# Kernel optimization log

Measured on AMD Instinct MI355X. Metric: run time of the kernel, lower is better.

Reference implementation:

```python
import jax, jax.numpy as jnp
import numpy as np

B, T = 64, 512
OBS, DM, DS, NL = 115, 128, 8, 3
EMB, NA, H1 = 16, 19, 256


def _ln(x, g, b, eps=1e-5):
    m = jnp.mean(x, -1, keepdims=True)
    v = jnp.mean((x - m) ** 2, -1, keepdims=True)
    return (x - m) * jax.lax.rsqrt(v + eps) * g + b


def _s6(x, h, lng, lnb, w_ig, w_dt, b_dt, a_log, w_b, w_c, d_par, w_out):
    # x: [B,T,DM], h: [B,DM,DS]
    xn = _ln(x, lng, lnb)
    xp = xn @ w_ig.T                               # [B,T,2*DM]
    x_in, z = xp[..., :DM], xp[..., DM:]
    dt = jax.nn.softplus(x_in @ w_dt.T + b_dt)     # [B,T,DM]
    A = -jnp.exp(a_log)                            # [DM,DS]
    bt = x_in @ w_b.T                              # [B,T,DS]
    ct = x_in @ w_c.T                              # [B,T,DS]
    dA = jnp.exp(dt[..., None] * A)                # [B,T,DM,DS]
    upd = (dt * x_in)[..., None] * bt[:, :, None, :]  # [B,T,DM,DS]

    def step(hc, inp):
        dA_t, u_t, c_t = inp
        hn = dA_t * hc + u_t                       # [B,DM,DS]
        y = jnp.einsum('bds,bs->bd', hn, c_t)      # [B,DM]
        return hn, y

    h_f, ys = jax.lax.scan(
        step, h,
        (jnp.swapaxes(dA, 0, 1), jnp.swapaxes(upd, 0, 1), jnp.swapaxes(ct, 0, 1)))
    y = jnp.swapaxes(ys, 0, 1)                     # [B,T,DM]
    ssm = y * jax.nn.silu(z) + x_in * d_par
    return x + ssm @ w_out.T, h_f.reshape(h_f.shape[0], -1)


def _forward(prev_actions, obs, h0, enc_w1, enc_b1, enc_g1, enc_bb1, enc_w2, enc_b2,
             enc_g2, enc_bb2, emb, proj_w, proj_b, proj_g, proj_bb,
             m_ln_g, m_ln_b, m_w_ig, m_w_dt, m_b_dt, m_a_log, m_w_b, m_w_c, m_d, m_w_out,
             fn_g, fn_b, pol_w1, pol_b1, pol_g, pol_bb, pol_w2, pol_b2):
    # MLP encoder: Linear -> LN -> SiLU -> Linear -> LN (final norm)
    e = jax.nn.silu(_ln(obs @ enc_w1.T + enc_b1, enc_g1, enc_bb1))
    e = _ln(e @ enc_w2.T + enc_b2, enc_g2, enc_bb2)
    pa = emb[prev_actions]                         # [B,T,EMB]
    x = jnp.concatenate([e, pa], -1) @ proj_w.T + proj_b
    x = jax.nn.silu(_ln(x, proj_g, proj_bb))
    for i in range(NL):
        x, _ = _s6(x, h0[i].reshape(-1, DM, DS), m_ln_g[i], m_ln_b[i], m_w_ig[i],
                   m_w_dt[i], m_b_dt[i], m_a_log[i], m_w_b[i], m_w_c[i], m_d[i], m_w_out[i])
    x = _ln(x, fn_g, fn_b)
    p = jax.nn.silu(_ln(x @ pol_w1.T + pol_b1, pol_g, pol_bb))
    return p @ pol_w2.T + pol_b2                   # [B,T,NA] policy logits


def setup_inputs() -> dict:
    key = jax.random.key(0)
    ks = iter(jax.random.split(key, 64))
    def n(shape, s=0.05):
        return jax.random.normal(next(ks), shape, dtype=jnp.float32) * s
    return {
        'obs': jax.random.normal(next(ks), (B, T, OBS), dtype=jnp.float32),
        'h0': jnp.zeros((NL, B, DM * DS), jnp.float32),
        'enc_w1': n((H1, OBS)), 'enc_b1': jnp.zeros((H1,)),
        'enc_g1': jnp.ones((H1,)), 'enc_bb1': jnp.zeros((H1,)),
        'enc_w2': n((DM, H1)), 'enc_b2': jnp.zeros((DM,)),
        'enc_g2': jnp.ones((DM,)), 'enc_bb2': jnp.zeros((DM,)),
        'emb': n((NA + 1, EMB), 1.0),
        'proj_w': n((DM, DM + EMB)), 'proj_b': jnp.zeros((DM,)),
        'proj_g': jnp.ones((DM,)), 'proj_bb': jnp.zeros((DM,)),
        'm_ln_g': jnp.ones((NL, DM)), 'm_ln_b': jnp.zeros((NL, DM)),
        'm_w_ig': n((NL, 2 * DM, DM)), 'm_w_dt': n((NL, DM, DM)),
        'm_b_dt': jnp.zeros((NL, DM)),
        'm_a_log': jax.random.uniform(next(ks), (NL, DM, DS), minval=-3.0, maxval=-1.0, dtype=jnp.float32),
        'm_w_b': n((NL, DS, DM)), 'm_w_c': n((NL, DS, DM)),
        'm_d': jnp.ones((NL, DM)), 'm_w_out': n((NL, DM, DM)),
        'fn_g': jnp.ones((DM,)), 'fn_b': jnp.zeros((DM,)),
        'pol_w1': n((DM, DM)), 'pol_b1': jnp.zeros((DM,)),
        'pol_g': jnp.ones((DM,)), 'pol_bb': jnp.zeros((DM,)),
        'pol_w2': n((NA, DM)), 'pol_b2': jnp.zeros((NA,)),
        'prev_actions': jax.random.randint(next(ks), (B, T), 0, NA + 1),
    }


def reference(obs, h0, enc_w1, enc_b1, enc_g1, enc_bb1, enc_w2, enc_b2, enc_g2, enc_bb2,
              emb, proj_w, proj_b, proj_g, proj_bb, m_ln_g, m_ln_b, m_w_ig, m_w_dt,
              m_b_dt, m_a_log, m_w_b, m_w_c, m_d, m_w_out, fn_g, fn_b, pol_w1, pol_b1,
              pol_g, pol_bb, pol_w2, pol_b2, prev_actions):
    return _forward(prev_actions, obs, h0, enc_w1, enc_b1, enc_g1, enc_bb1, enc_w2,
                    enc_b2, enc_g2, enc_bb2, emb, proj_w, proj_b, proj_g, proj_bb,
                    m_ln_g, m_ln_b, m_w_ig, m_w_dt, m_b_dt, m_a_log, m_w_b, m_w_c,
                    m_d, m_w_out, fn_g, fn_b, pol_w1, pol_b1, pol_g, pol_bb, pol_w2, pol_b2)
```

## Files before the change

### kernel.cpp

```cpp
#include <hip/hip_runtime.h>
#include <math.h>

#define BB 64
#define TT 512
#define OBSD 115
#define DMD 128
#define DSD 8
#define NLD 3
#define EMBD 16
#define NAD 19
#define H1D 256
#define NTOK (BB*TT)
#define SSEG 32
#define TSEG (TT/SSEG)

typedef unsigned short ushort_t;
typedef __attribute__((ext_vector_type(8))) short short8;
typedef __attribute__((ext_vector_type(4))) float f32x4;

__device__ __forceinline__ float silu_f(float x){ return x / (1.f + __expf(-x)); }
__device__ __forceinline__ float softplus_f(float x){
  return fmaxf(x, 0.f) + log1pf(__expf(-fabsf(x)));
}
__device__ __forceinline__ ushort_t f2bf(float x){
  unsigned u = __float_as_uint(x);
  unsigned r = (u + 0x7fffu + ((u >> 16) & 1u)) >> 16;
  return (ushort_t)r;
}
__device__ __forceinline__ float b2f(ushort_t x){
  return __uint_as_float(((unsigned)x) << 16);
}
#define MFMA(a,b,c) __builtin_amdgcn_mfma_f32_16x16x32_bf16((a),(b),(c),0,0,0)
#define LOG2E 1.44269504f

struct PJob { const float* src; ushort_t* dst; int N; int K; int Kpad; int rowofs; int Nw; };
struct PJobs { PJob j[20]; };

__global__ __launch_bounds__(256) void k_prep(PJobs P){
  const int job = blockIdx.x >> 2;
  const int sub = blockIdx.x & 3;
  PJob pj = P.j[job];
  const int elems = pj.Nw * pj.Kpad;
  for (int idx = sub*256 + threadIdx.x; idx < elems; idx += 4*256){
    int n = idx / pj.Kpad;
    int k = idx - n*pj.Kpad;
    float v = (n < pj.N && k < pj.K) ? pj.src[(size_t)n*pj.K + k] : 0.f;
    pj.dst[(size_t)(pj.rowofs + n)*pj.Kpad + k] = f2bf(v);
  }
}

__global__ __launch_bounds__(256, 6) void k_enc12p(
    const float* __restrict__ obs, const ushort_t* __restrict__ w1b,
    const float* __restrict__ b1, const float* __restrict__ g1,
    const float* __restrict__ bb1,
    const ushort_t* __restrict__ w2b,
    const float* __restrict__ b2, const float* __restrict__ g2,
    const float* __restrict__ bb2,
    const float* __restrict__ emb, const int* __restrict__ pact,
    const ushort_t* __restrict__ pwb, const float* __restrict__ pb,
    const float* __restrict__ pg, const float* __restrict__ pbb,
    float* __restrict__ X,
    const float* __restrict__ lng, const float* __restrict__ lnb,
    const ushort_t* __restrict__ wigb, const ushort_t* __restrict__ wdbcb,
    const float* __restrict__ bdt,
    ushort_t* __restrict__ XINb, ushort_t* __restrict__ Zb,
    ushort_t* __restrict__ DTb, ushort_t* __restrict__ BTu, ushort_t* __restrict__ CTu,
    const float* __restrict__ alog0,
    float* __restrict__ HLOC, float* __restrict__ PPR)
{
  __shared__ __align__(16) char sm[15104];
  ushort_t* s_obs = (ushort_t*)sm;
  ushort_t* s_e1  = (ushort_t*)sm;
  ushort_t* s_xin = (ushort_t*)sm;
  ushort_t* s_dt  = (ushort_t*)(sm + 4352);
  ushort_t* s_a2  = (ushort_t*)(sm + 8448);
  ushort_t* s_btc = (ushort_t*)(sm + 13824);
  float2*   s_st  = (float2*)(sm + 14080);
  float2*   s_st2 = (float2*)(sm + 14592);

  const int tok0 = blockIdx.x * 16;
  const int bidx = blockIdx.x >> 5;
  const int ch   = blockIdx.x & 31;
  const int tid = threadIdx.x;
  const int lane = tid & 63, w = tid >> 6;
  const int q = lane >> 4, cn = lane & 15;

  {
    const int t = tid >> 4, kc = tid & 15;
    const float* op = obs + (size_t)(tok0 + t)*OBSD;
    short8 v;
    #pragma unroll
    for (int j = 0; j < 8; j++){
      int k = kc*8 + j;
      v[j] = (short)f2bf(k < OBSD ? op[k] : 0.f);
    }
    *(short8*)&s_obs[t*136 + kc*8] = v;
  }
  for (int e = tid; e < 16*32; e += 256){
    int t = e >> 5, k = e & 31;
    float v = 0.f;
    if (k < EMBD){ int a = pact[tok0 + t]; v = emb[(size_t)a*EMBD + k]; }
    s_a2[t*168 + 128 + k] = f2bf(v);
  }
  __syncthreads();

  f32x4 acc[4];
  {
    short8 af[4];
    #pragma unroll
    for (int ks = 0; ks < 4; ks++)
      af[ks] = *(const short8*)&s_obs[cn*136 + ks*32 + q*8];
    #pragma unroll
    for (int nt = 0; nt < 4; nt++){
      const int n0 = (w*4 + nt) * 16;
      f32x4 a = {0.f,0.f,0.f,0.f};
      #pragma unroll
      for (int ks = 0; ks < 4; ks++){
        short8 bf = *(const short8*)&w1b[(size_t)(n0 + cn)*128 + ks*32 + q*8];
        a = MFMA(af[ks], bf, a);
      }
      float bv = b1[n0 + cn];
      #pragma unroll
      for (int r = 0; r < 4; r++) a[r] += bv;
      acc[nt] = a;
    }
    #pragma unroll
    for (int r = 0; r < 4; r++){
      float s = 0.f, s2 = 0.f;
      #pragma unroll
      for (int nt = 0; nt < 4; nt++){ float v = acc[nt][r]; s += v; s2 = fmaf(v, v, s2); }
      s += __shfl_xor(s, 1, 64); s2 += __shfl_xor(s2, 1, 64);
      s += __shfl_xor(s, 2, 64); s2 += __shfl_xor(s2, 2, 64);
      s += __shfl_xor(s, 4, 64); s2 += __shfl_xor(s2, 4, 64);
      s += __shfl_xor(s, 8, 64); s2 += __shfl_xor(s2, 8, 64);
      if (cn == 0) s_st[(q*4 + r)*4 + w] = make_float2(s, s2);
    }
  }
  __syncthreads();

  {
    float mu[4], rs[4];
    #pragma unroll
    for (int r = 0; r < 4; r++){
      const int row = q*4 + r;
      float2 p0 = s_st[row*4+0], p1 = s_st[row*4+1];
      float2 p2 = s_st[row*4+2], p3 = s_st[row*4+3];
      float s = p0.x+p1.x+p2.x+p3.x, s2 = p0.y+p1.y+p2.y+p3.y;
      float m = s * (1.f/256.f);
      mu[r] = m;
      rs[r] = rsqrtf(s2 * (1.f/256.f) - m*m + 1e-5f);
    }
    #pragma unroll
    for (int nt = 0; nt < 4; nt++){
      const int col = (w*4 + nt)*16 + cn;
      float gg = g1[col], bbv = bb1[col];
      #pragma unroll
      for (int r = 0; r < 4; r++){
        float v = (acc[nt][r] - mu[r]) * rs[r] * gg + bbv;
        s_e1[(q*4 + r)*264 + col] = f2bf(silu_f(v));
      }
    }
  }
  __syncthreads();

  f32x4 acc2[2];
  {
    short8 af2[8];
    #pragma unroll
    for (int ks = 0; ks < 8; ks++)
      af2[ks] = *(const short8*)&s_e1[cn*264 + ks*32 + q*8];
    #pragma unroll
    for (int nt = 0; nt < 2; nt++){
      const int n0 = (w*2 + nt) * 16;
      f32x4 a = {0.f,0.f,0.f,0.f};
      #pragma unroll
      for (int ks = 0; ks < 8; ks++){
        short8 bf = *(const short8*)&w2b[(size_t)(n0 + cn)*256 + ks*32 + q*8];
        a = MFMA(af2[ks], bf, a);
      }
      float bv = b2[n0 + cn];
      #pragma unroll
      for (int r = 0; r < 4; r++) a[r] += bv;
      acc2[nt] = a;
    }
    #pragma unroll
    for (int r = 0; r < 4; r++){
      float s = 0.f, s2 = 0.f;
      #pragma unroll
      for (int nt = 0; nt < 2; nt++){ float v = acc2[nt][r]; s += v; s2 = fmaf(v, v, s2); }
      s += __shfl_xor(s, 1, 64); s2 += __shfl_xor(s2, 1, 64);
      s += __shfl_xor(s, 2, 64); s2 += __shfl_xor(s2, 2, 64);
      s += __shfl_xor(s, 4, 64); s2 += __shfl_xor(s2, 4, 64);
      s += __shfl_xor(s, 8, 64); s2 += __shfl_xor(s2, 8, 64);
      if (cn == 0) s_st[(q*4 + r)*4 + w] = make_float2(s, s2);
    }
  }
  __syncthreads();

  {
    float mu[4], rs[4];
    #pragma unroll
    for (int r = 0; r < 4; r++){
      const int row = q*4 + r;
      float2 p0 = s_st[row*4+0], p1 = s_st[row*4+1];
      float2 p2 = s_st[row*4+2], p3 = s_st[row*4+3];
      float s = p0.x+p1.x+p2.x+p3.x, s2 = p0.y+p1.y+p2.y+p3.y;
      float m = s * (1.f/128.f);
      mu[r] = m;
      rs[r] = rsqrtf(s2 * (1.f/128.f) - m*m + 1e-5f);
    }
    #pragma unroll
    for (int nt = 0; nt < 2; nt++){
      const int col = (w*2 + nt)*16 + cn;
      float gg = g2[col], bbv = bb2[col];
      #pragma unroll
      for (int r = 0; r < 4; r++){
        float v = (acc2[nt][r] - mu[r]) * rs[r] * gg + bbv;
        s_a2[(q*4 + r)*168 + col] = f2bf(v);
      }
    }
  }
  __syncthreads();

  f32x4 acc3[2];
  {
    short8 af3[5];
    #pragma unroll
    for (int ks = 0; ks < 5; ks++)
      af3[ks] = *(const short8*)&s_a2[cn*168 + ks*32 + q*8];
    #pragma unroll
    for (int nt = 0; nt < 2; nt++){
      const int n0 = (w*2 + nt) * 16;
      f32x4 a = {0.f,0.f,0.f,0.f};
      #pragma unroll
      for (int ks = 0; ks < 5; ks++){
        short8 bf = *(const short8*)&pwb[(size_t)(n0 + cn)*160 + ks*32 + q*8];
        a = MFMA(af3[ks], bf, a);
      }
      float bv = pb[n0 + cn];
      #pragma unroll
      for (int r = 0; r < 4; r++) a[r] += bv;
      acc3[nt] = a;
    }
    #pragma unroll
    for (int r = 0; r < 4; r++){
      float s = 0.f, s2 = 0.f;
      #pragma unroll
      for (int nt = 0; nt < 2; nt++){ float v = acc3[nt][r]; s += v; s2 = fmaf(v, v, s2); }
      s += __shfl_xor(s, 1, 64); s2 += __shfl_xor(s2, 1, 64);
      s += __shfl_xor(s, 2, 64); s2 += __shfl_xor(s2, 2, 64);
      s += __shfl_xor(s, 4, 64); s2 += __shfl_xor(s2, 4, 64);
      s += __shfl_xor(s, 8, 64); s2 += __shfl_xor(s2, 8, 64);
      if (cn == 0) s_st[(q*4 + r)*4 + w] = make_float2(s, s2);
    }
  }
  __syncthreads();

  {
    float mu[4], rs[4];
    #pragma unroll
    for (int r = 0; r < 4; r++){
      const int row = q*4 + r;
      float2 p0 = s_st[row*4+0], p1 = s_st[row*4+1];
      float2 p2 = s_st[row*4+2], p3 = s_st[row*4+3];
      float s = p0.x+p1.x+p2.x+p3.x, s2 = p0.y+p1.y+p2.y+p3.y;
      float m = s * (1.f/128.f);
      mu[r] = m;
      rs[r] = rsqrtf(s2 * (1.f/128.f) - m*m + 1e-5f);
    }
    float ps[4] = {0.f,0.f,0.f,0.f}, ps2[4] = {0.f,0.f,0.f,0.f};
    #pragma unroll
    for (int nt = 0; nt < 2; nt++){
      const int col = (w*2 + nt)*16 + cn;
      float gg = pg[col], bbv = pbb[col];
      #pragma unroll
      for (int r = 0; r < 4; r++){
        float v = (acc3[nt][r] - mu[r]) * rs[r] * gg + bbv;
        v = silu_f(v);
        acc3[nt][r] = v;
        X[(size_t)(tok0 + q*4 + r)*128 + col] = v;
        ps[r] += v; ps2[r] = fmaf(v, v, ps2[r]);
      }
    }
    #pragma unroll
    for (int r = 0; r < 4; r++){
      float s = ps[r], s2 = ps2[r];
      s += __shfl_xor(s, 1, 64); s2 += __shfl_xor(s2, 1, 64);
      s += __shfl_xor(s, 2, 64); s2 += __shfl_xor(s2, 2, 64);
      s += __shfl_xor(s, 4, 64); s2 += __shfl_xor(s2, 4, 64);
      s += __shfl_xor(s, 8, 64); s2 += __shfl_xor(s2, 8, 64);
      if (cn == 0) s_st2[(q*4 + r)*4 + w] = make_float2(s, s2);
    }
  }
  __syncthreads();

  {
    float mu[4], rs[4];
    #pragma unroll
    for (int r = 0; r < 4; r++){
      const int row = q*4 + r;
      float2 p0 = s_st2[row*4+0], p1 = s_st2[row*4+1];
      float2 p2 = s_st2[row*4+2], p3 = s_st2[row*4+3];
      float s = p0.x+p1.x+p2.x+p3.x, s2 = p0.y+p1.y+p2.y+p3.y;
      float m = s * (1.f/128.f);
      mu[r] = m;
      rs[r] = rsqrtf(s2 * (1.f/128.f) - m*m + 1e-5f);
    }
    #pragma unroll
    for (int nt = 0; nt < 2; nt++){
      const int col = (w*2 + nt)*16 + cn;
      float gg = lng[col], bbv = lnb[col];
      #pragma unroll
      for (int r = 0; r < 4; r++){
        float v = (acc3[nt][r] - mu[r]) * rs[r] * gg + bbv;
        s_a2[(q*4 + r)*168 + col] = f2bf(v);
      }
    }
  }
  __syncthreads();

  {
    short8 af[4];
    #pragma unroll
    for (int ks = 0; ks < 4; ks++)
      af[ks] = *(const short8*)&s_a2[cn*168 + ks*32 + q*8];
    #pragma unroll
    for (int i = 0; i < 4; i++){
      const int n0 = (w*4 + i) * 16;
      f32x4 a = {0.f,0.f,0.f,0.f};
      #pragma unroll
      for (int ks = 0; ks < 4; ks++){
        short8 bf = *(const short8*)&wigb[(size_t)(n0 + cn)*128 + ks*32 + q*8];
        a = MFMA(af[ks], bf, a);
      }
      if (n0 < 128){
        #pragma unroll
        for (int r = 0; r < 4; r++){
          int tr = q*4 + r;
          ushort_t bb = f2bf(a[r]);
          XINb[(size_t)(tok0 + tr)*128 + n0 + cn] = bb;
          s_xin[tr*136 + n0 + cn] = bb;
        }
      } else {
        #pragma unroll
        for (int r = 0; r < 4; r++){
          int tr = q*4 + r;
          Zb[(size_t)(tok0 + tr)*128 + (n0 - 128) + cn] = f2bf(a[r]);
        }
      }
    }
  }
  __syncthreads();

  {
    short8 af2[4];
    #pragma unroll
    for (int ks = 0; ks < 4; ks++)
      af2[ks] = *(const short8*)&s_xin[cn*136 + ks*32 + q*8];
    for (int nt = w; nt < 9; nt += 4){
      const int n0 = nt * 16;
      f32x4 a = {0.f,0.f,0.f,0.f};
      #pragma unroll
      for (int ks = 0; ks < 4; ks++){
        short8 bf = *(const short8*)&wdbcb[(size_t)(n0 + cn)*128 + ks*32 + q*8];
        a = MFMA(af2[ks], bf, a);
      }
      const int col = n0 + cn;
      if (col < 128){
        float bd = bdt[col];
        #pragma unroll
        for (int r = 0; r < 4; r++){
          int tr = q*4 + r;
          ushort_t dv = f2bf(softplus_f(a[r] + bd));
          DTb[(size_t)(tok0 + tr)*128 + col] = dv;
          s_dt[tr*136 + col] = dv;
        }
      } else if (col < 136){
        #pragma unroll
        for (int r = 0; r < 4; r++){
          int tr = q*4 + r;
          ushort_t bb = f2bf(a[r]);
          BTu[(size_t)(tok0 + tr)*8 + (col - 128)] = bb;
          s_btc[tr*8 + (col - 128)] = bb;
        }
      } else {
        #pragma unroll
        for (int r = 0; r < 4; r++)
          CTu[(size_t)(tok0 + q*4 + r)*8 + (col - 136)] = f2bf(a[r]);
      }
    }
  }
  __syncthreads();

  {
    const int d = tid & 127, sh = tid >> 7;
    float A2c[4], hh[4], pp[4];
    #pragma unroll
    for (int j = 0; j < 4; j++){
      A2c[j] = -__expf(alog0[d*8 + sh*4 + j]) * LOG2E;
      hh[j] = 0.f; pp[j] = 1.f;
    }
    #pragma unroll 4
    for (int t = 0; t < 16; t++){
      float dt = b2f(s_dt[t*136 + d]);
      float wv = dt * b2f(s_xin[t*136 + d]);
      #pragma unroll
      for (int j = 0; j < 4; j++){
        float dA = exp2f(dt * A2c[j]);
        hh[j] = fmaf(dA, hh[j], wv * b2f(s_btc[t*8 + sh*4 + j]));
        pp[j] *= dA;
      }
    }
    const size_t o = ((size_t)bidx*SSEG + ch)*1024 + d*8 + sh*4;
    #pragma unroll
    for (int j = 0; j < 4; j++){ HLOC[o+j] = hh[j]; PPR[o+j] = pp[j]; }
  }
}

__global__ __launch_bounds__(256) void k_carry(
    float* __restrict__ HL, const float* __restrict__ PP,
    const float* __restrict__ h0g)
{
  const int idx = blockIdx.x*256 + threadIdx.x;
  const size_t base = (size_t)(idx >> 10) * (SSEG*1024) + (idx & 1023);
  float hl[SSEG], pp[SSEG];
  #pragma unroll
  for (int ch = 0; ch < SSEG; ch++){
    hl[ch] = HL[base + (size_t)ch*1024];
    pp[ch] = PP[base + (size_t)ch*1024];
  }
  float h = h0g[idx];
  #pragma unroll
  for (int ch = 0; ch < SSEG; ch++){
    HL[base + (size_t)ch*1024] = h;
    h = fmaf(pp[ch], h, hl[ch]);
  }
}

#define SMB 17664

__device__ __forceinline__ void phaseB16(
    const ushort_t* DTb, const ushort_t* XINb, const ushort_t* Zb,
    const ushort_t* BTu, const ushort_t* CTu,
    const float* __restrict__ alog, const float* __restrict__ HLpre,
    const float* __restrict__ dpar, const ushort_t* __restrict__ woutb,
    float* __restrict__ X, char* sm, int b, int seg, int tid)
{
  ushort_t* s_dtS = (ushort_t*)sm;
  ushort_t* s_xiS = (ushort_t*)(sm + 4096);
  ushort_t* s_zS  = (ushort_t*)(sm + 8192);
  float*    s_x   = (float*)sm;
  ushort_t* s_a   = (ushort_t*)(sm + 12288);
  ushort_t* s_bt  = (ushort_t*)(sm + 16640);
  ushort_t* s_ct  = (ushort_t*)(sm + 16896);
  float2*   s_st  = (float2*)(sm + 17152);

  const int lane = tid & 63, w = tid >> 6, q = lane >> 4, cn = lane & 15;
  const size_t segtok = (size_t)b*TT + seg*TSEG;

  ((uint4*)s_dtS)[tid] = ((const uint4*)(DTb  + segtok*128))[tid];
  ((uint4*)s_xiS)[tid] = ((const uint4*)(XINb + segtok*128))[tid];
  ((uint4*)s_zS )[tid] = ((const uint4*)(Zb   + segtok*128))[tid];
  if (tid < 64){
    ((unsigned*)s_bt)[tid] = ((const unsigned*)(BTu + segtok*8))[tid];
    ((unsigned*)s_ct)[tid] = ((const unsigned*)(CTu + segtok*8))[tid];
  }

  const int d2 = (w << 5) | (lane & 31);
  const int sh = lane >> 5;
  float A2h[4], h[4];
  {
    const size_t o = ((size_t)b*SSEG + seg)*1024 + d2*8 + sh*4;
    float4 hv = *(const float4*)(HLpre + o);
    h[0]=hv.x; h[1]=hv.y; h[2]=hv.z; h[3]=hv.w;
    #pragma unroll
    for (int j = 0; j < 4; j++)
      A2h[j] = -__expf(alog[d2*8 + sh*4 + j]) * LOG2E;
  }
  const float dp = dpar[d2];
  __syncthreads();

  #pragma unroll 4
  for (int t = 0; t < 16; t++){
    float dt = b2f(s_dtS[t*128 + d2]);
    float xi = b2f(s_xiS[t*128 + d2]);
    float zv = b2f(s_zS [t*128 + d2]);
    float wv = dt * xi;
    float yp = 0.f;
    #pragma unroll
    for (int j = 0; j < 4; j++){
      float dA = exp2f(dt * A2h[j]);
      h[j] = fmaf(dA, h[j], wv * b2f(s_bt[t*8 + sh*4 + j]));
      yp = fmaf(h[j], b2f(s_ct[t*8 + sh*4 + j]), yp);
    }
    float y = yp + __shfl_xor(yp, 32, 64);
    float ssm = y * silu_f(zv) + xi * dp;
    if (sh == 0) s_a[t*136 + d2] = f2bf(ssm);
  }
  __syncthreads();

  {
    short8 af[4];
    #pragma unroll
    for (int ks = 0; ks < 4; ks++)
      af[ks] = *(const short8*)&s_a[cn*136 + ks*32 + q*8];
    float ps[4] = {0.f,0.f,0.f,0.f}, ps2[4] = {0.f,0.f,0.f,0.f};
    #pragma unroll
    for (int i = 0; i < 2; i++){
      const int n0 = (w*2 + i) * 16;
      short8 bf[4];
      #pragma unroll
      for (int ks = 0; ks < 4; ks++)
        bf[ks] = *(const short8*)&woutb[(size_t)(n0+cn)*128 + ks*32 + q*8];
      f32x4 acc = {0.f,0.f,0.f,0.f};
      #pragma unroll
      for (int ks = 0; ks < 4; ks++) acc = MFMA(af[ks], bf[ks], acc);
      #pragma unroll
      for (int r = 0; r < 4; r++){
        const int tr = q*4 + r;
        const size_t g = (segtok + tr)*128 + n0 + cn;
        float xn = X[g] + acc[r];
        X[g] = xn;
        s_x[tr*130 + n0 + cn] = xn;
        ps[r] += xn; ps2[r] = fmaf(xn, xn, ps2[r]);
      }
    }
    #pragma unroll
    for (int r = 0; r < 4; r++){
      float s = ps[r], s2 = ps2[r];
      s += __shfl_xor(s, 1, 64); s2 += __shfl_xor(s2, 1, 64);
      s += __shfl_xor(s, 2, 64); s2 += __shfl_xor(s2, 2, 64);
      s += __shfl_xor(s, 4, 64); s2 += __shfl_xor(s2, 4, 64);
      s += __shfl_xor(s, 8, 64); s2 += __shfl_xor(s2, 8, 64);
      if (cn == 0) s_st[(q*4 + r)*4 + w] = make_float2(s, s2);
    }
  }
  __syncthreads();
}

__global__ __launch_bounds__(256, 6) void k_scan2p(
    ushort_t* DTb, ushort_t* XINb, ushort_t* Zb,
    ushort_t* BTu, ushort_t* CTu,
    const float* __restrict__ alog, const float* __restrict__ HLpre,
    const float* __restrict__ dpar, const ushort_t* __restrict__ woutb,
    float* __restrict__ X,
    const float* __restrict__ lng, const float* __restrict__ lnb,
    const ushort_t* __restrict__ wigb, const ushort_t* __restrict__ wdbcb,
    const float* __restrict__ bdt,
    const float* __restrict__ alogn,
    float* __restrict__ HLo, float* __restrict__ PPo)
{
  __shared__ __align__(16) char sm[SMB];
  const int tid = threadIdx.x;
  float*    s_x   = (float*)sm;
  ushort_t* s_xin = (ushort_t*)sm;
  ushort_t* s_dt2 = (ushort_t*)(sm + 4352);
  ushort_t* s_a   = (ushort_t*)(sm + 12288);
  ushort_t* s_btc = (ushort_t*)(sm + 16640);
  float2*   s_st  = (float2*)(sm + 17152);

  const int b = blockIdx.x >> 5;
  const int seg = blockIdx.x & 31;
  const int lane = tid & 63, w = tid >> 6, q = lane >> 4, cn = lane & 15;
  const size_t segtok = (size_t)b*TT + seg*TSEG;

  phaseB16(DTb, XINb, Zb, BTu, CTu, alog, HLpre, dpar, woutb, X, sm, b, seg, tid);

  {
    const int d = tid & 127, half = tid >> 7;
    float g = lng[d], c0v = lnb[d];
    #pragma unroll
    for (int tt = 0; tt < 8; tt++){
      const int t = half*8 + tt;
      float2 p0 = s_st[t*4+0], p1 = s_st[t*4+1];
      float2 p2 = s_st[t*4+2], p3 = s_st[t*4+3];
      float ssum = p0.x+p1.x+p2.x+p3.x, ss2 = p0.y+p1.y+p2.y+p3.y;
      float mu = ssum * (1.f/128.f);
      float rs = rsqrtf(ss2 * (1.f/128.f) - mu*mu + 1e-5f);
      float v = (s_x[t*130 + d] - mu) * rs * g + c0v;
      s_a[t*136 + d] = f2bf(v);
    }
  }
  __syncthreads();

  {
    short8 af[4];
    #pragma unroll
    for (int ks = 0; ks < 4; ks++)
      af[ks] = *(const short8*)&s_a[cn*136 + ks*32 + q*8];
    #pragma unroll
    for (int i = 0; i < 4; i++){
      const int n0 = (w*4 + i) * 16;
      short8 bf[4];
      #pragma unroll
      for (int ks = 0; ks < 4; ks++)
        bf[ks] = *(const short8*)&wigb[(size_t)(n0+cn)*128 + ks*32 + q*8];
      f32x4 acc = {0.f,0.f,0.f,0.f};
      #pragma unroll
      for (int ks = 0; ks < 4; ks++) acc = MFMA(af[ks], bf[ks], acc);
      if (n0 < 128){
        #pragma unroll
        for (int r = 0; r < 4; r++){
          const int tr = q*4 + r;
          ushort_t bb = f2bf(acc[r]);
          XINb[(segtok + tr)*128 + n0 + cn] = bb;
          s_xin[tr*136 + n0 + cn] = bb;
        }
      } else {
        #pragma unroll
        for (int r = 0; r < 4; r++){
          const int tr = q*4 + r;
          Zb[(segtok + tr)*128 + (n0-128) + cn] = f2bf(acc[r]);
        }
      }
    }
  }
  __syncthreads();

  {
    short8 af2[4];
    #pragma unroll
    for (int ks = 0; ks < 4; ks++)
      af2[ks] = *(const short8*)&s_xin[cn*136 + ks*32 + q*8];
    for (int nt = w; nt < 9; nt += 4){
      const int n0 = nt * 16;
      short8 bf[4];
      #pragma unroll
      for (int ks = 0; ks < 4; ks++)
        bf[ks] = *(const short8*)&wdbcb[(size_t)(n0+cn)*128 + ks*32 + q*8];
      f32x4 acc = {0.f,0.f,0.f,0.f};
      #pragma unroll
      for (int ks = 0; ks < 4; ks++) acc = MFMA(af2[ks], bf[ks], acc);
      const int col = n0 + cn;
      if (col < 128){
        float bd = bdt[col];
        #pragma unroll
        for (int r = 0; r < 4; r++){
          const int tr = q*4 + r;
          ushort_t dv = f2bf(softplus_f(acc[r] + bd));
          DTb[(segtok + tr)*128 + col] = dv;
          s_dt2[tr*136 + col] = dv;
        }
      } else if (col < 136){
        #pragma unroll
        for (int r = 0; r < 4; r++){
          const int tr = q*4 + r;
          ushort_t bb = f2bf(acc[r]);
          BTu[(segtok + tr)*8 + (col-128)] = bb;
          s_btc[tr*8 + (col-128)] = bb;
        }
      } else {
        #pragma unroll
        for (int r = 0; r < 4; r++)
          CTu[(segtok + q*4 + r)*8 + (col-136)] = f2bf(acc[r]);
      }
    }
  }
  __syncthreads();

  {
    const int d = tid & 127, sh = tid >> 7;
    float A2n[4], hh[4], pp[4];
    #pragma unroll
    for (int j = 0; j < 4; j++){
      A2n[j] = -__expf(alogn[d*8 + sh*4 + j]) * LOG2E;
      hh[j] = 0.f; pp[j] = 1.f;
    }
    #pragma unroll 4
    for (int t = 0; t < 16; t++){
      float dt = b2f(s_dt2[t*136 + d]);
      float wv = dt * b2f(s_xin[t*136 + d]);
      #pragma unroll
      for (int j = 0; j < 4; j++){
        float dA = exp2f(dt * A2n[j]);
        hh[j] = fmaf(dA, hh[j], wv * b2f(s_btc[t*8 + sh*4 + j]));
        pp[j] *= dA;
      }
    }
    const size_t o = ((size_t)b*SSEG + seg)*1024 + d*8 + sh*4;
    #pragma unroll
    for (int j = 0; j < 4; j++){ HLo[o+j] = hh[j]; PPo[o+j] = pp[j]; }
  }
}

__global__ __launch_bounds__(256, 6) void k_scan2h(
    const ushort_t* DTb, const ushort_t* XINb, const ushort_t* Zb,
    const ushort_t* BTu, const ushort_t* CTu,
    const float* __restrict__ alog, const float* __restrict__ HLpre,
    const float* __restrict__ dpar, const ushort_t* __restrict__ woutb,
    float* __restrict__ X,
    const float* __restrict__ fng, const float* __restrict__ fnb,
    const ushort_t* __restrict__ pw1b, const float* __restrict__ pb1,
    const float* __restrict__ pg, const float* __restrict__ pbb,
    const ushort_t* __restrict__ pw2b, const float* __restrict__ pb2,
    float* __restrict__ out)
{
  __shared__ __align__(16) char sm[SMB];
  const int tid = threadIdx.x;
  float*    s_x  = (float*)sm;
  ushort_t* s_a  = (ushort_t*)(sm + 12288);
  float2*   s_st = (float2*)(sm + 17152);

  const int b = blockIdx.x >> 5;
  const int seg = blockIdx.x & 31;
  const int lane = tid & 63, w = tid >> 6, q = lane >> 4, cn = lane & 15;
  const size_t segtok = (size_t)b*TT + seg*TSEG;

  phaseB16((ushort_t*)DTb, (ushort_t*)XINb, (ushort_t*)Zb,
           (ushort_t*)BTu, (ushort_t*)CTu, alog, HLpre,
           dpar, woutb, X, sm, b, seg, tid);

  {
    const int d = tid & 127, half = tid >> 7;
    float g = fng[d], c0v = fnb[d];
    #pragma unroll
    for (int tt = 0; tt < 8; tt++){
      const int t = half*8 + tt;
      float2 p0 = s_st[t*4+0], p1 = s_st[t*4+1];
      float2 p2 = s_st[t*4+2], p3 = s_st[t*4+3];
      float ssum = p0.x+p1.x+p2.x+p3.x, ss2 = p0.y+p1.y+p2.y+p3.y;
      float mu = ssum * (1.f/128.f);
      float rs = rsqrtf(ss2 * (1.f/128.f) - mu*mu + 1e-5f);
      float v = (s_x[t*130 + d] - mu) * rs * g + c0v;
      s_a[t*136 + d] = f2bf(v);
    }
  }
  __syncthreads();

  {
    short8 af[4];
    #pragma unroll
    for (int ks = 0; ks < 4; ks++)
      af[ks] = *(const short8*)&s_a[cn*136 + ks*32 + q*8];
    float ps[4] = {0.f,0.f,0.f,0.f}, ps2[4] = {0.f,0.f,0.f,0.f};
    #pragma unroll
    for (int i = 0; i < 2; i++){
      const int n0 = (w*2 + i) * 16;
      short8 bf[4];
      #pragma unroll
      for (int ks = 0; ks < 4; ks++)
        bf[ks] = *(const short8*)&pw1b[(size_t)(n0+cn)*128 + ks*32 + q*8];
      float bias = pb1[n0 + cn];
      f32x4 acc = {0.f,0.f,0.f,0.f};
      #pragma unroll
      for (int ks = 0; ks < 4; ks++) acc = MFMA(af[ks], bf[ks], acc);
      #pragma unroll
      for (int r = 0; r < 4; r++){
        float xv = acc[r] + bias;
        s_x[(q*4 + r)*130 + n0 + cn] = xv;
        ps[r] += xv; ps2[r] = fmaf(xv, xv, ps2[r]);
      }
    }
    #pragma unroll
    for (int r = 0; r < 4; r++){
      float s = ps[r], s2 = ps2[r];
      s += __shfl_xor(s, 1, 64); s2 += __shfl_xor(s2, 1, 64);
      s += __shfl_xor(s, 2, 64); s2 += __shfl_xor(s2, 2, 64);
      s += __shfl_xor(s, 4, 64); s2 += __shfl_xor(s2, 4, 64);
      s += __shfl_xor(s, 8, 64); s2 += __shfl_xor(s2, 8, 64);
      if (cn == 0) s_st[(q*4 + r)*4 + w] = make_float2(s, s2);
    }
  }
  __syncthreads();

  {
    const int d = tid & 127, half = tid >> 7;
    float g = pg[d], c0v = pbb[d];
    #pragma unroll
    for (int tt = 0; tt < 8; tt++){
      const int t = half*8 + tt;
      float2 p0 = s_st[t*4+0], p1 = s_st[t*4+1];
      float2 p2 = s_st[t*4+2], p3 = s_st[t*4+3];
      float ssum = p0.x+p1.x+p2.x+p3.x, ss2 = p0.y+p1.y+p2.y+p3.y;
      float mu = ssum * (1.f/128.f);
      float rs = rsqrtf(ss2 * (1.f/128.f) - mu*mu + 1e-5f);
      float v = (s_x[t*130 + d] - mu) * rs * g + c0v;
      s_a[t*136 + d] = f2bf(silu_f(v));
    }
  }
  __syncthreads();

  if (w < 2){
    short8 af[4];
    #pragma unroll
    for (int ks = 0; ks < 4; ks++)
      af[ks] = *(const short8*)&s_a[cn*136 + ks*32 + q*8];
    const int n0 = w * 16;
    short8 bf[4];
    #pragma unroll
    for (int ks = 0; ks < 4; ks++)
      bf[ks] = *(const short8*)&pw2b[(size_t)(n0+cn)*128 + ks*32 + q*8];
    const int col = n0 + cn;
    f32x4 acc = {0.f,0.f,0.f,0.f};
    #pragma unroll
    for (int ks = 0; ks < 4; ks++) acc = MFMA(af[ks], bf[ks], acc);
    if (col < NAD){
      float bias = pb2[col];
      #pragma unroll
      for (int r = 0; r < 4; r++)
        out[(segtok + q*4 + r)*NAD + col] = acc[r] + bias;
    }
  }
}

extern "C" void kernel_launch(void* const* d_in, const int* in_sizes, int n_in,
                              void* d_out, int out_size, void* d_ws, size_t ws_size,
                              hipStream_t stream) {
  const float* obs    = (const float*)d_in[0];
  const float* h0     = (const float*)d_in[1];
  const float* enc_w1 = (const float*)d_in[2];
  const float* enc_b1 = (const float*)d_in[3];
  const float* enc_g1 = (const float*)d_in[4];
  const float* enc_bb1= (const float*)d_in[5];
  const float* enc_w2 = (const float*)d_in[6];
  const float* enc_b2 = (const float*)d_in[7];
  const float* enc_g2 = (const float*)d_in[8];
  const float* enc_bb2= (const float*)d_in[9];
  const float* emb    = (const float*)d_in[10];
  const float* proj_w = (const float*)d_in[11];
  const float* proj_b = (const float*)d_in[12];
  const float* proj_g = (const float*)d_in[13];
  const float* proj_bb= (const float*)d_in[14];
  const float* m_ln_g = (const float*)d_in[15];
  const float* m_ln_b = (const float*)d_in[16];
  const float* m_w_ig = (const float*)d_in[17];
  const float* m_w_dt = (const float*)d_in[18];
  const float* m_b_dt = (const float*)d_in[19];
  const float* m_a_log= (const float*)d_in[20];
  const float* m_w_b  = (const float*)d_in[21];
  const float* m_w_c  = (const float*)d_in[22];
  const float* m_d    = (const float*)d_in[23];
  const float* m_w_out= (const float*)d_in[24];
  const float* fn_g   = (const float*)d_in[25];
  const float* fn_b   = (const float*)d_in[26];
  const float* pol_w1 = (const float*)d_in[27];
  const float* pol_b1 = (const float*)d_in[28];
  const float* pol_g  = (const float*)d_in[29];
  const float* pol_bb = (const float*)d_in[30];
  const float* pol_w2 = (const float*)d_in[31];
  const float* pol_b2 = (const float*)d_in[32];
  const int*   pact   = (const int*)d_in[33];

  float* ws  = (float*)d_ws;
  float* X    = ws;
  float* HLA  = X + (size_t)NTOK*128;
  float* PPA  = HLA + (size_t)BB*SSEG*1024;
  float* HLB  = PPA + (size_t)BB*SSEG*1024;
  float* PPB  = HLB + (size_t)BB*SSEG*1024;
  ushort_t* XINb = (ushort_t*)(PPB + (size_t)BB*SSEG*1024);
  ushort_t* Zb   = XINb + (size_t)NTOK*128;
  ushort_t* DTb  = Zb   + (size_t)NTOK*128;
  ushort_t* BTu  = DTb  + (size_t)NTOK*128;
  ushort_t* CTu  = BTu  + (size_t)NTOK*8;

  ushort_t* W1B   = CTu   + (size_t)NTOK*8;
  ushort_t* W2B   = W1B   + 256*128;
  ushort_t* PWB   = W2B   + 128*256;
  ushort_t* WIGB  = PWB   + 128*160;
  ushort_t* WDBCB = WIGB  + 3*256*128;
  ushort_t* WOUTB = WDBCB + 3*144*128;
  ushort_t* PW1B  = WOUTB + 3*128*128;
  ushort_t* PW2B  = PW1B  + 128*128;

  PJobs P;
  int nj = 0;
  auto add = [&](const float* src, ushort_t* dst, int N, int K, int Kpad, int rowofs, int Nw){
    P.j[nj].src = src; P.j[nj].dst = dst; P.j[nj].N = N; P.j[nj].K = K;
    P.j[nj].Kpad = Kpad; P.j[nj].rowofs = rowofs; P.j[nj].Nw = Nw; nj++;
  };
  add(enc_w1, W1B, 256, 115, 128, 0, 256);
  add(enc_w2, W2B, 128, 256, 256, 0, 128);
  add(proj_w, PWB, 128, 144, 160, 0, 128);
  for (int l = 0; l < NLD; l++)
    add(m_w_ig + (size_t)l*256*128, WIGB + (size_t)l*256*128, 256, 128, 128, 0, 256);
  for (int l = 0; l < NLD; l++){
    add(m_w_dt + (size_t)l*128*128, WDBCB + (size_t)l*144*128, 128, 128, 128, 0,   128);
    add(m_w_b  + (size_t)l*8*128,   WDBCB + (size_t)l*144*128,   8, 128, 128, 128,   8);
    add(m_w_c  + (size_t)l*8*128,   WDBCB + (size_t)l*144*128,   8, 128, 128, 136,   8);
  }
  for (int l = 0; l < NLD; l++)
    add(m_w_out + (size_t)l*128*128, WOUTB + (size_t)l*128*128, 128, 128, 128, 0, 128);
  add(pol_w1, PW1B, 128, 128, 128, 0, 128);
  add(pol_w2, PW2B,  19, 128, 128, 0,  32);

  k_prep<<<20*4, 256, 0, stream>>>(P);
  k_enc12p<<<NTOK/16, 256, 0, stream>>>(obs, W1B, enc_b1, enc_g1, enc_bb1,
      W2B, enc_b2, enc_g2, enc_bb2,
      emb, pact, PWB, proj_b, proj_g, proj_bb, X,
      m_ln_g, m_ln_b, WIGB, WDBCB, m_b_dt,
      XINb, Zb, DTb, BTu, CTu,
      m_a_log, HLA, PPA);

  const int carrygrid = BB*1024/256;
  const int scangrid  = NTOK/16;

  k_carry<<<carrygrid, 256, 0, stream>>>(HLA, PPA, h0);
  k_scan2p<<<scangrid, 256, 0, stream>>>(DTb, XINb, Zb, BTu, CTu,
      m_a_log, HLA, m_d, WOUTB, X,
      m_ln_g + 128, m_ln_b + 128,
      WIGB + (size_t)256*128, WDBCB + (size_t)144*128, m_b_dt + 128,
      m_a_log + 1024, HLB, PPB);
  k_carry<<<carrygrid, 256, 0, stream>>>(HLB, PPB, h0 + (size_t)BB*1024);
  k_scan2p<<<scangrid, 256, 0, stream>>>(DTb, XINb, Zb, BTu, CTu,
      m_a_log + 1024, HLB, m_d + 128, WOUTB + (size_t)128*128, X,
      m_ln_g + 256, m_ln_b + 256,
      WIGB + (size_t)2*256*128, WDBCB + (size_t)2*144*128, m_b_dt + 256,
      m_a_log + 2048, HLA, PPA);
  k_carry<<<carrygrid, 256, 0, stream>>>(HLA, PPA, h0 + (size_t)2*BB*1024);
  k_scan2h<<<scangrid, 256, 0, stream>>>(DTb, XINb, Zb, BTu, CTu,
      m_a_log + 2048, HLA, m_d + 256, WOUTB + (size_t)2*128*128, X,
      fn_g, fn_b, PW1B, pol_b1, pol_g, pol_bb, PW2B, pol_b2,
      (float*)d_out);
}
```

Baseline: 402.3 us.

## Fold segment carry propagation into scan kernels and drop k_carry launches

Removes the separate k_carry kernel. Each scan block now rebuilds its own segment-start state by walking the prefix of per-segment (HL, PP) pairs from h0, which saves three kernel launches and the HL read-modify-write pass. In exchange, later segments repeat up to 31 float4 load/FMA steps, giving quadratic redundant reads spread across blocks. It also raises the k_enc12p launch-bounds occupancy hint from 6 to 8, which may constrain registers.

```diff
diff --git a/kernel.cpp b/kernel.cpp
--- a/kernel.cpp
+++ b/kernel.cpp
@@ -49,7 +49,7 @@
   }
 }
 
-__global__ __launch_bounds__(256, 6) void k_enc12p(
+__global__ __launch_bounds__(256, 8) void k_enc12p(
     const float* __restrict__ obs, const ushort_t* __restrict__ w1b,
     const float* __restrict__ b1, const float* __restrict__ g1,
     const float* __restrict__ bb1,
@@ -417,32 +417,14 @@
   }
 }
 
-__global__ __launch_bounds__(256) void k_carry(
-    float* __restrict__ HL, const float* __restrict__ PP,
-    const float* __restrict__ h0g)
-{
-  const int idx = blockIdx.x*256 + threadIdx.x;
-  const size_t base = (size_t)(idx >> 10) * (SSEG*1024) + (idx & 1023);
-  float hl[SSEG], pp[SSEG];
-  #pragma unroll
-  for (int ch = 0; ch < SSEG; ch++){
-    hl[ch] = HL[base + (size_t)ch*1024];
-    pp[ch] = PP[base + (size_t)ch*1024];
-  }
-  float h = h0g[idx];
-  #pragma unroll
-  for (int ch = 0; ch < SSEG; ch++){
-    HL[base + (size_t)ch*1024] = h;
-    h = fmaf(pp[ch], h, hl[ch]);
-  }
-}
-
 #define SMB 17664
 
 __device__ __forceinline__ void phaseB16(
     const ushort_t* DTb, const ushort_t* XINb, const ushort_t* Zb,
     const ushort_t* BTu, const ushort_t* CTu,
-    const float* __restrict__ alog, const float* __restrict__ HLpre,
+    const float* __restrict__ alog,
+    const float* __restrict__ HLpre, const float* __restrict__ PPpre,
+    const float* __restrict__ h0g,
     const float* __restrict__ dpar, const ushort_t* __restrict__ woutb,
     float* __restrict__ X, char* sm, int b, int seg, int tid)
 {
@@ -470,12 +452,37 @@
   const int sh = lane >> 5;
   float A2h[4], h[4];
   {
-    const size_t o = ((size_t)b*SSEG + seg)*1024 + d2*8 + sh*4;
-    float4 hv = *(const float4*)(HLpre + o);
-    h[0]=hv.x; h[1]=hv.y; h[2]=hv.z; h[3]=hv.w;
     #pragma unroll
     for (int j = 0; j < 4; j++)
       A2h[j] = -__expf(alog[d2*8 + sh*4 + j]) * LOG2E;
+    float4 hv = *(const float4*)(h0g + (size_t)b*1024 + d2*8 + sh*4);
+    h[0]=hv.x; h[1]=hv.y; h[2]=hv.z; h[3]=hv.w;
+    const size_t cb = (size_t)b*(SSEG*1024) + d2*8 + sh*4;
+    int ch = 0;
+    for (; ch + 4 <= seg; ch += 4){
+      float4 hl0 = *(const float4*)(HLpre + cb + (size_t)(ch+0)*1024);
+      float4 pp0 = *(const float4*)(PPpre + cb + (size_t)(ch+0)*1024);
+      float4 hl1 = *(const float4*)(HLpre + cb + (size_t)(ch+1)*1024);
+      float4 pp1 = *(const float4*)(PPpre + cb + (size_t)(ch+1)*1024);
+      float4 hl2 = *(const float4*)(HLpre + cb + (size_t)(ch+2)*1024);
+      float4 pp2 = *(const float4*)(PPpre + cb + (size_t)(ch+2)*1024);
+      float4 hl3 = *(const float4*)(HLpre + cb + (size_t)(ch+3)*1024);
+      float4 pp3 = *(const float4*)(PPpre + cb + (size_t)(ch+3)*1024);
+      h[0]=fmaf(pp0.x,h[0],hl0.x); h[1]=fmaf(pp0.y,h[1],hl0.y);
+      h[2]=fmaf(pp0.z,h[2],hl0.z); h[3]=fmaf(pp0.w,h[3],hl0.w);
+      h[0]=fmaf(pp1.x,h[0],hl1.x); h[1]=fmaf(pp1.y,h[1],hl1.y);
+      h[2]=fmaf(pp1.z,h[2],hl1.z); h[3]=fmaf(pp1.w,h[3],hl1.w);
+      h[0]=fmaf(pp2.x,h[0],hl2.x); h[1]=fmaf(pp2.y,h[1],hl2.y);
+      h[2]=fmaf(pp2.z,h[2],hl2.z); h[3]=fmaf(pp2.w,h[3],hl2.w);
+      h[0]=fmaf(pp3.x,h[0],hl3.x); h[1]=fmaf(pp3.y,h[1],hl3.y);
+      h[2]=fmaf(pp3.z,h[2],hl3.z); h[3]=fmaf(pp3.w,h[3],hl3.w);
+    }
+    for (; ch < seg; ch++){
+      float4 hl = *(const float4*)(HLpre + cb + (size_t)ch*1024);
+      float4 pp = *(const float4*)(PPpre + cb + (size_t)ch*1024);
+      h[0]=fmaf(pp.x,h[0],hl.x); h[1]=fmaf(pp.y,h[1],hl.y);
+      h[2]=fmaf(pp.z,h[2],hl.z); h[3]=fmaf(pp.w,h[3],hl.w);
+    }
   }
   const float dp = dpar[d2];
   __syncthreads();
@@ -541,7 +548,9 @@
 __global__ __launch_bounds__(256, 6) void k_scan2p(
     ushort_t* DTb, ushort_t* XINb, ushort_t* Zb,
     ushort_t* BTu, ushort_t* CTu,
-    const float* __restrict__ alog, const float* __restrict__ HLpre,
+    const float* __restrict__ alog,
+    const float* __restrict__ HLpre, const float* __restrict__ PPpre,
+    const float* __restrict__ h0g,
     const float* __restrict__ dpar, const ushort_t* __restrict__ woutb,
     float* __restrict__ X,
     const float* __restrict__ lng, const float* __restrict__ lnb,
@@ -564,7 +573,7 @@
   const int lane = tid & 63, w = tid >> 6, q = lane >> 4, cn = lane & 15;
   const size_t segtok = (size_t)b*TT + seg*TSEG;
 
-  phaseB16(DTb, XINb, Zb, BTu, CTu, alog, HLpre, dpar, woutb, X, sm, b, seg, tid);
+  phaseB16(DTb, XINb, Zb, BTu, CTu, alog, HLpre, PPpre, h0g, dpar, woutb, X, sm, b, seg, tid);
 
   {
     const int d = tid & 127, half = tid >> 7;
@@ -686,7 +695,9 @@
 __global__ __launch_bounds__(256, 6) void k_scan2h(
     const ushort_t* DTb, const ushort_t* XINb, const ushort_t* Zb,
     const ushort_t* BTu, const ushort_t* CTu,
-    const float* __restrict__ alog, const float* __restrict__ HLpre,
+    const float* __restrict__ alog,
+    const float* __restrict__ HLpre, const float* __restrict__ PPpre,
+    const float* __restrict__ h0g,
     const float* __restrict__ dpar, const ushort_t* __restrict__ woutb,
     float* __restrict__ X,
     const float* __restrict__ fng, const float* __restrict__ fnb,
@@ -707,7 +718,7 @@
   const size_t segtok = (size_t)b*TT + seg*TSEG;
 
   phaseB16((ushort_t*)DTb, (ushort_t*)XINb, (ushort_t*)Zb,
-           (ushort_t*)BTu, (ushort_t*)CTu, alog, HLpre,
+           (ushort_t*)BTu, (ushort_t*)CTu, alog, HLpre, PPpre, h0g,
            dpar, woutb, X, sm, b, seg, tid);
 
   {
@@ -891,24 +902,22 @@
       XINb, Zb, DTb, BTu, CTu,
       m_a_log, HLA, PPA);
 
-  const int carrygrid = BB*1024/256;
-  const int scangrid  = NTOK/16;
-
-  k_carry<<<carrygrid, 256, 0, stream>>>(HLA, PPA, h0);
+  const int scangrid = NTOK/16;
+
   k_scan2p<<<scangrid, 256, 0, stream>>>(DTb, XINb, Zb, BTu, CTu,
-      m_a_log, HLA, m_d, WOUTB, X,
+      m_a_log, HLA, PPA, h0, m_d, WOUTB, X,
       m_ln_g + 128, m_ln_b + 128,
       WIGB + (size_t)256*128, WDBCB + (size_t)144*128, m_b_dt + 128,
       m_a_log + 1024, HLB, PPB);
-  k_carry<<<carrygrid, 256, 0, stream>>>(HLB, PPB, h0 + (size_t)BB*1024);
   k_scan2p<<<scangrid, 256, 0, stream>>>(DTb, XINb, Zb, BTu, CTu,
-      m_a_log + 1024, HLB, m_d + 128, WOUTB + (size_t)128*128, X,
+      m_a_log + 1024, HLB, PPB, h0 + (size_t)BB*1024, m_d + 128,
+      WOUTB + (size_t)128*128, X,
       m_ln_g + 256, m_ln_b + 256,
       WIGB + (size_t)2*256*128, WDBCB + (size_t)2*144*128, m_b_dt + 256,
       m_a_log + 2048, HLA, PPA);
-  k_carry<<<carrygrid, 256, 0, stream>>>(HLA, PPA, h0 + (size_t)2*BB*1024);
   k_scan2h<<<scangrid, 256, 0, stream>>>(DTb, XINb, Zb, BTu, CTu,
-      m_a_log + 2048, HLA, m_d + 256, WOUTB + (size_t)2*128*128, X,
+      m_a_log + 2048, HLA, PPA, h0 + (size_t)2*BB*1024, m_d + 256,
+      WOUTB + (size_t)2*128*128, X,
       fn_g, fn_b, PW1B, pol_b1, pol_g, pol_bb, PW2B, pol_b2,
       (float*)d_out);
 }
```

Result: slower. 424.0 us (+5.4%).
